# Kernel optimization log

Hardware: AMD Instinct MI355X
Metric: run time of the kernel (lower is better)

## Reference

```python
import jax, jax.numpy as jnp
import numpy as np

B, D, O = 512, 256, 256
H = [512, 1024, 1024]

def _linear_params(key, fan_in, fan_out):
    kw, kb = jax.random.split(key)
    bound = 1.0 / np.sqrt(fan_in)
    W = jax.random.uniform(kw, (fan_out, fan_in), jnp.float32, -bound, bound)
    b = jax.random.uniform(kb, (fan_out,), jnp.float32, -bound, bound)
    return W, b

def setup_inputs() -> dict:
    key = jax.random.key(0)
    ks = jax.random.split(key, 7)
    input_values = jax.random.normal(ks[0], (B, D), jnp.float32)
    nan_flag = jax.random.uniform(ks[1], (B, D), jnp.float32)
    W_in, b_in = _linear_params(ks[2], D, H[0])          # input_layer: nan_flag_dim -> H[0]
    W_h1, b_h1 = _linear_params(ks[3], H[0], H[1])        # hidden layer 1
    W_h2, b_h2 = _linear_params(ks[4], H[1], H[2])        # hidden layer 2
    W_d, b_d = _linear_params(ks[5], H[2], D * O)         # output_branch_dense
    W_b, b_b = _linear_params(ks[6], H[2], O)             # output_branch_bias
    return {"input_values": input_values, "nan_flag": nan_flag, "training": False,
            "W_in": W_in, "b_in": b_in, "W_h1": W_h1, "b_h1": b_h1,
            "W_h2": W_h2, "b_h2": b_h2, "W_d": W_d, "b_d": b_d,
            "W_b": W_b, "b_b": b_b}

def reference(input_values, nan_flag, training, W_in, b_in, W_h1, b_h1, W_h2, b_h2, W_d, b_d, W_b, b_b):
    # training=False: dropout is identity, sample_missing branch skipped (default False)
    x = jax.nn.relu(nan_flag @ W_in.T + b_in)
    x = jax.nn.relu(x @ W_h1.T + b_h1)
    x = jax.nn.relu(x @ W_h2.T + b_h2)
    # per-sample compensation weights [B, D, O] and bias [B, O]
    comp_w = (x @ W_d.T + b_d).reshape(B, D, O)
    comp_b = x @ W_b.T + b_b
    # baddbmm: [B,1,D] @ [B,D,O] + [B,1,O] -> squeeze -> [B,O]
    out = comp_b + jnp.einsum('bd,bdo->bo', input_values, comp_w)
    return out
```

## Files before the change

### kernel.cpp

```cpp
#include <hip/hip_runtime.h>

#define B_  512
#define D_  256
#define O_  256
#define H2_ 1024

typedef __attribute__((ext_vector_type(4))) float  f32x4;
typedef __attribute__((ext_vector_type(8))) short  short8;
typedef __attribute__((ext_vector_type(4))) short  short4v;
typedef unsigned short ushort_t;

union S8u  { short4v v; unsigned u[2]; };
union S16u { short8  v; unsigned u[4]; };

__device__ __forceinline__ unsigned f32_bf16(float x) {
  unsigned u = __builtin_bit_cast(unsigned, x);
  return (u + 0x7fffu + ((u >> 16) & 1u)) >> 16;
}
__device__ __forceinline__ unsigned cvt_pk_bf16(float a, float b) {
  return f32_bf16(a) | (f32_bf16(b) << 16);
}

__device__ __forceinline__ void gload_lds16(const void* g, void* l) {
  __builtin_amdgcn_global_load_lds(
      (const __attribute__((address_space(1))) unsigned*)g,
      (__attribute__((address_space(3))) unsigned*)l, 16, 0, 0);
}

template <int RELU>
__global__ __launch_bounds__(256)
void gemm_bt64(const float* __restrict__ A, const float* __restrict__ Bm,
               const float* __restrict__ bias, float* __restrict__ C,
               int M, int N, int K) {
  __shared__ __align__(16) short As[64][72];
  __shared__ __align__(16) short Bs[64][72];
  const int t    = threadIdx.x;
  const int m0   = blockIdx.y * 64;
  const int n0   = blockIdx.x * 64;
  const int f4c  = t & 15;
  const int rg   = t >> 4;
  const int lane = t & 63;
  const int w    = t >> 6;
  const int wm   = (w & 1) * 32;
  const int wn   = (w >> 1) * 32;
  const int lr   = lane & 15;
  const int lq   = lane >> 4;

  f32x4 acc[2][2];
  #pragma unroll
  for (int i = 0; i < 2; ++i)
    #pragma unroll
    for (int j = 0; j < 2; ++j) acc[i][j] = f32x4{0.f, 0.f, 0.f, 0.f};

  for (int k0 = 0; k0 < K; k0 += 64) {
    #pragma unroll
    for (int j = 0; j < 4; ++j) {
      int r = rg + 16 * j;
      f32x4 av = *(const f32x4*)(A  + (size_t)(m0 + r) * K + k0 + f4c * 4);
      f32x4 bv = *(const f32x4*)(Bm + (size_t)(n0 + r) * K + k0 + f4c * 4);
      S8u sa; sa.u[0] = cvt_pk_bf16(av.x, av.y); sa.u[1] = cvt_pk_bf16(av.z, av.w);
      S8u sb; sb.u[0] = cvt_pk_bf16(bv.x, bv.y); sb.u[1] = cvt_pk_bf16(bv.z, bv.w);
      *(short4v*)&As[r][f4c * 4] = sa.v;
      *(short4v*)&Bs[r][f4c * 4] = sb.v;
    }
    __syncthreads();
    #pragma unroll
    for (int ks = 0; ks < 2; ++ks) {
      short8 a0 = *(const short8*)&As[wm + lr     ][ks * 32 + lq * 8];
      short8 a1 = *(const short8*)&As[wm + 16 + lr][ks * 32 + lq * 8];
      short8 b0 = *(const short8*)&Bs[wn + lr     ][ks * 32 + lq * 8];
      short8 b1 = *(const short8*)&Bs[wn + 16 + lr][ks * 32 + lq * 8];
      acc[0][0] = __builtin_amdgcn_mfma_f32_16x16x32_bf16(a0, b0, acc[0][0], 0, 0, 0);
      acc[0][1] = __builtin_amdgcn_mfma_f32_16x16x32_bf16(a0, b1, acc[0][1], 0, 0, 0);
      acc[1][0] = __builtin_amdgcn_mfma_f32_16x16x32_bf16(a1, b0, acc[1][0], 0, 0, 0);
      acc[1][1] = __builtin_amdgcn_mfma_f32_16x16x32_bf16(a1, b1, acc[1][1], 0, 0, 0);
    }
    __syncthreads();
  }
  #pragma unroll
  for (int mi = 0; mi < 2; ++mi)
    #pragma unroll
    for (int ni = 0; ni < 2; ++ni)
      #pragma unroll
      for (int r = 0; r < 4; ++r) {
        int row = m0 + wm + mi * 16 + lq * 4 + r;
        int col = n0 + wn + ni * 16 + lr;
        float v = acc[mi][ni][r] + bias[col];
        if (RELU) v = fmaxf(v, 0.f);
        C[(size_t)row * N + col] = v;
      }
}

__global__ __launch_bounds__(256)
void cvt_f32_bf16(const float* __restrict__ in, ushort_t* __restrict__ out, int n8) {
  for (size_t i = (size_t)blockIdx.x * 256 + threadIdx.x; i < (size_t)n8;
       i += (size_t)gridDim.x * 256) {
    const float* p = in + i * 8;
    f32x4 v0 = *(const f32x4*)p;
    f32x4 v1 = *(const f32x4*)(p + 4);
    S16u s;
    s.u[0] = cvt_pk_bf16(v0.x, v0.y);
    s.u[1] = cvt_pk_bf16(v0.z, v0.w);
    s.u[2] = cvt_pk_bf16(v1.x, v1.y);
    s.u[3] = cvt_pk_bf16(v1.z, v1.w);
    *(short8*)(out + i * 8) = s.v;
  }
}

__global__ __launch_bounds__(256, 3)
void stage_b5(const ushort_t* __restrict__ x2b, const float* __restrict__ inp,
              const float* __restrict__ Wd, const float* __restrict__ bd,
              float* __restrict__ out) {
  __shared__ __align__(16) ushort_t As[2][128 * 32];
  __shared__ __align__(16) ushort_t Bs[2][128 * 32];
  const int t    = threadIdx.x;
  const int x    = blockIdx.x;
  const int q    = blockIdx.y;
  const int mt   = q & 3;
  const int nb   = (q >> 2) * 8 + x;
  const int d0   = (nb >> 4) * 8;
  const int og   = (nb & 15) * 16;
  const int bm   = mt * 128;
  const int lane = t & 63;
  const int w    = t >> 6;
  const int wm   = (w >> 1) * 64;
  const int wn   = (w & 1) * 64;
  const int lr   = lane & 15;
  const int lq   = lane >> 4;

  const int arow = lane >> 2;
  const int aswz = (lane & 3) ^ ((arow >> 1) & 3);
  const ushort_t* aptr[2];
  #pragma unroll
  for (int c = 0; c < 2; ++c)
    aptr[c] = x2b + (size_t)(bm + w * 32 + c * 16 + arow) * H2_ + aswz * 8;

  const int rr = t >> 1;
  const int hh = t & 1;
  const int wr = (d0 + (rr >> 4)) * O_ + og + (rr & 15);
  const float* bptr = Wd + (size_t)wr * H2_ + hh * 16;
  const int bsw = (rr >> 1) & 3;

  const int sl = (lq ^ ((lr >> 1) & 3)) * 8;

  f32x4 acc[4][4];
  #pragma unroll
  for (int mi = 0; mi < 4; ++mi)
    #pragma unroll
    for (int nj = 0; nj < 4; ++nj) acc[mi][nj] = f32x4{0.f, 0.f, 0.f, 0.f};

  f32x4 breg[4];

  auto stageA = [&](int k, int bf) {
    #pragma unroll
    for (int c = 0; c < 2; ++c)
      gload_lds16(aptr[c] + k * 32, &As[bf][(w * 32 + c * 16) * 32]);
  };
  auto loadB = [&](int k) {
    const float* p = bptr + k * 32;
    breg[0] = *(const f32x4*)p;
    breg[1] = *(const f32x4*)(p + 4);
    breg[2] = *(const f32x4*)(p + 8);
    breg[3] = *(const f32x4*)(p + 12);
  };
  auto writeB = [&](int bf) {
    S16u s0, s1;
    s0.u[0] = cvt_pk_bf16(breg[0].x, breg[0].y);
    s0.u[1] = cvt_pk_bf16(breg[0].z, breg[0].w);
    s0.u[2] = cvt_pk_bf16(breg[1].x, breg[1].y);
    s0.u[3] = cvt_pk_bf16(breg[1].z, breg[1].w);
    s1.u[0] = cvt_pk_bf16(breg[2].x, breg[2].y);
    s1.u[1] = cvt_pk_bf16(breg[2].z, breg[2].w);
    s1.u[2] = cvt_pk_bf16(breg[3].x, breg[3].y);
    s1.u[3] = cvt_pk_bf16(breg[3].z, breg[3].w);
    const int lcg0 = hh * 2;
    *(short8*)&Bs[bf][rr * 32 + (lcg0 ^ bsw) * 8]       = s0.v;
    *(short8*)&Bs[bf][rr * 32 + ((lcg0 + 1) ^ bsw) * 8] = s1.v;
  };

  stageA(0, 0);
  loadB(0);
  asm volatile("s_waitcnt vmcnt(0)" ::: "memory");
  writeB(0);
  asm volatile("s_waitcnt lgkmcnt(0)" ::: "memory");
  __builtin_amdgcn_s_barrier();

  int buf = 0;
  for (int k = 0; k < 32; ++k) {
    if (k < 31) {
      stageA(k + 1, buf ^ 1);
      loadB(k + 1);
    }

    short8 af[4], bfv[4];
    #pragma unroll
    for (int mi = 0; mi < 4; ++mi)
      af[mi] = *(const short8*)&As[buf][(wm + mi * 16 + lr) * 32 + sl];
    #pragma unroll
    for (int nj = 0; nj < 4; ++nj)
      bfv[nj] = *(const short8*)&Bs[buf][(wn + nj * 16 + lr) * 32 + sl];
    #pragma unroll
    for (int mi = 0; mi < 4; ++mi)
      #pragma unroll
      for (int nj = 0; nj < 4; ++nj)
        acc[mi][nj] = __builtin_amdgcn_mfma_f32_16x16x32_bf16(af[mi], bfv[nj],
                                                              acc[mi][nj], 0, 0, 0);

    if (k < 31) {
      asm volatile("s_waitcnt vmcnt(0)" ::: "memory");
      writeB(buf ^ 1);
      asm volatile("s_waitcnt lgkmcnt(0)" ::: "memory");
      __builtin_amdgcn_s_barrier();
      buf ^= 1;
    }
  }

  const int dbase = d0 + (w & 1) * 4;
  const int o     = og + lr;
  float bdv[4];
  #pragma unroll
  for (int nj = 0; nj < 4; ++nj)
    bdv[nj] = bd[(size_t)(dbase + nj) * O_ + o];
  #pragma unroll
  for (int mi = 0; mi < 4; ++mi)
    #pragma unroll
    for (int r = 0; r < 4; ++r) {
      const int row = bm + wm + mi * 16 + lq * 4 + r;
      f32x4 sc = *(const f32x4*)(inp + (size_t)row * D_ + dbase);
      float v = sc.x * (acc[mi][0][r] + bdv[0]) +
                sc.y * (acc[mi][1][r] + bdv[1]) +
                sc.z * (acc[mi][2][r] + bdv[2]) +
                sc.w * (acc[mi][3][r] + bdv[3]);
      atomicAdd(out + (size_t)row * O_ + o, v);
    }
}

extern "C" void kernel_launch(void* const* d_in, const int* in_sizes, int n_in,
                              void* d_out, int out_size, void* d_ws, size_t ws_size,
                              hipStream_t stream) {
  const float* input = (const float*)d_in[0];
  const float* nanf  = (const float*)d_in[1];
  const float* W_in  = (const float*)d_in[3];
  const float* b_in  = (const float*)d_in[4];
  const float* W_h1  = (const float*)d_in[5];
  const float* b_h1  = (const float*)d_in[6];
  const float* W_h2  = (const float*)d_in[7];
  const float* b_h2  = (const float*)d_in[8];
  const float* W_d   = (const float*)d_in[9];
  const float* b_d   = (const float*)d_in[10];
  const float* W_b   = (const float*)d_in[11];
  const float* b_b   = (const float*)d_in[12];
  float* out = (float*)d_out;

  float* x0 = (float*)d_ws;
  float* x1 = x0 + 512 * 512;
  float* x2 = x1 + 512 * 1024;
  ushort_t* x2b = (ushort_t*)(x2 + 512 * 1024);

  gemm_bt64<1><<<dim3(512 / 64, 512 / 64), 256, 0, stream>>>(nanf, W_in, b_in, x0, 512, 512, 256);
  gemm_bt64<1><<<dim3(1024 / 64, 512 / 64), 256, 0, stream>>>(x0, W_h1, b_h1, x1, 512, 1024, 512);
  gemm_bt64<1><<<dim3(1024 / 64, 512 / 64), 256, 0, stream>>>(x1, W_h2, b_h2, x2, 512, 1024, 1024);
  cvt_f32_bf16<<<256, 256, 0, stream>>>(x2, x2b, 512 * 1024 / 8);
  gemm_bt64<0><<<dim3(256 / 64, 512 / 64), 256, 0, stream>>>(x2, W_b, b_b, out, 512, 256, 1024);
  stage_b5<<<dim3(8, 256), 256, 0, stream>>>(x2b, input, W_d, b_d, out);
}
```

Measured before the change: 584.1 us.

## Deepen W_d prefetch and replace atomics with partial buffers plus reduction

The main stage_b kernel now prefetches W_d tiles two k-steps ahead and writes them to LDS before the MFMA loop instead of after it, so global load latency overlaps with compute. The per-element atomicAdd epilogue is replaced by an in-block LDS reduction across the two d-halves, followed by plain stores into 32 partial buffers indexed by d-group. A new reduce_parts kernel sums those partials into the output. Occupancy hint rises from 3 to 4 blocks per SM. The trade-off is extra register pressure from the deeper prefetch, a 16 MB partial workspace, and one more kernel launch.

```diff
diff --git a/kernel.cpp b/kernel.cpp
--- a/kernel.cpp
+++ b/kernel.cpp
@@ -107,10 +107,10 @@
   }
 }
 
-__global__ __launch_bounds__(256, 3)
-void stage_b5(const ushort_t* __restrict__ x2b, const float* __restrict__ inp,
+__global__ __launch_bounds__(256, 4)
+void stage_b6(const ushort_t* __restrict__ x2b, const float* __restrict__ inp,
               const float* __restrict__ Wd, const float* __restrict__ bd,
-              float* __restrict__ out) {
+              float* __restrict__ part) {
   __shared__ __align__(16) ushort_t As[2][128 * 32];
   __shared__ __align__(16) ushort_t Bs[2][128 * 32];
   const int t    = threadIdx.x;
@@ -118,7 +118,8 @@
   const int q    = blockIdx.y;
   const int mt   = q & 3;
   const int nb   = (q >> 2) * 8 + x;
-  const int d0   = (nb >> 4) * 8;
+  const int dg   = nb >> 4;
+  const int d0   = dg * 8;
   const int og   = (nb & 15) * 16;
   const int bm   = mt * 128;
   const int lane = t & 63;
@@ -181,7 +182,9 @@
   stageA(0, 0);
   loadB(0);
   asm volatile("s_waitcnt vmcnt(0)" ::: "memory");
+  __builtin_amdgcn_sched_barrier(0);
   writeB(0);
+  loadB(1);
   asm volatile("s_waitcnt lgkmcnt(0)" ::: "memory");
   __builtin_amdgcn_s_barrier();
 
@@ -189,7 +192,10 @@
   for (int k = 0; k < 32; ++k) {
     if (k < 31) {
       stageA(k + 1, buf ^ 1);
-      loadB(k + 1);
+      asm volatile("s_waitcnt vmcnt(2)" ::: "memory");
+      __builtin_amdgcn_sched_barrier(0);
+      writeB(buf ^ 1);
+      if (k < 30) loadB(k + 2);
     }
 
     short8 af[4], bfv[4];
@@ -207,13 +213,14 @@
                                                               acc[mi][nj], 0, 0, 0);
 
     if (k < 31) {
-      asm volatile("s_waitcnt vmcnt(0)" ::: "memory");
-      writeB(buf ^ 1);
+      if (k < 30) { asm volatile("s_waitcnt vmcnt(4)" ::: "memory"); }
+      else        { asm volatile("s_waitcnt vmcnt(0)" ::: "memory"); }
       asm volatile("s_waitcnt lgkmcnt(0)" ::: "memory");
       __builtin_amdgcn_s_barrier();
       buf ^= 1;
     }
   }
+  __builtin_amdgcn_sched_barrier(0);
 
   const int dbase = d0 + (w & 1) * 4;
   const int o     = og + lr;
@@ -221,18 +228,54 @@
   #pragma unroll
   for (int nj = 0; nj < 4; ++nj)
     bdv[nj] = bd[(size_t)(dbase + nj) * O_ + o];
+
+  float v[4][4];
   #pragma unroll
   for (int mi = 0; mi < 4; ++mi)
     #pragma unroll
     for (int r = 0; r < 4; ++r) {
       const int row = bm + wm + mi * 16 + lq * 4 + r;
       f32x4 sc = *(const f32x4*)(inp + (size_t)row * D_ + dbase);
-      float v = sc.x * (acc[mi][0][r] + bdv[0]) +
-                sc.y * (acc[mi][1][r] + bdv[1]) +
-                sc.z * (acc[mi][2][r] + bdv[2]) +
-                sc.w * (acc[mi][3][r] + bdv[3]);
-      atomicAdd(out + (size_t)row * O_ + o, v);
-    }
+      v[mi][r] = sc.x * (acc[mi][0][r] + bdv[0]) +
+                 sc.y * (acc[mi][1][r] + bdv[1]) +
+                 sc.z * (acc[mi][2][r] + bdv[2]) +
+                 sc.w * (acc[mi][3][r] + bdv[3]);
+    }
+
+  __syncthreads();
+  float* lf = (float*)As;
+  if (w & 1) {
+    #pragma unroll
+    for (int mi = 0; mi < 4; ++mi)
+      #pragma unroll
+      for (int r = 0; r < 4; ++r) {
+        const int rl = wm + mi * 16 + lq * 4 + r;
+        lf[rl * 17 + lr] = v[mi][r];
+      }
+  }
+  __syncthreads();
+  if (!(w & 1)) {
+    float* pb = part + (size_t)dg * (B_ * O_);
+    #pragma unroll
+    for (int mi = 0; mi < 4; ++mi)
+      #pragma unroll
+      for (int r = 0; r < 4; ++r) {
+        const int rl = wm + mi * 16 + lq * 4 + r;
+        pb[(size_t)(bm + rl) * O_ + o] = v[mi][r] + lf[rl * 17 + lr];
+      }
+  }
+}
+
+__global__ __launch_bounds__(256)
+void reduce_parts(const float* __restrict__ part, float* __restrict__ out) {
+  const int b = blockIdx.x;
+  const int o = threadIdx.x;
+  const size_t idx = (size_t)b * O_ + o;
+  float s = 0.f;
+  #pragma unroll 8
+  for (int j = 0; j < 32; ++j)
+    s += part[(size_t)j * (B_ * O_) + idx];
+  out[idx] += s;
 }
 
 extern "C" void kernel_launch(void* const* d_in, const int* in_sizes, int n_in,
@@ -256,11 +299,13 @@
   float* x1 = x0 + 512 * 512;
   float* x2 = x1 + 512 * 1024;
   ushort_t* x2b = (ushort_t*)(x2 + 512 * 1024);
+  float* part = (float*)((char*)d_ws + 8ull * 1024 * 1024);
 
   gemm_bt64<1><<<dim3(512 / 64, 512 / 64), 256, 0, stream>>>(nanf, W_in, b_in, x0, 512, 512, 256);
   gemm_bt64<1><<<dim3(1024 / 64, 512 / 64), 256, 0, stream>>>(x0, W_h1, b_h1, x1, 512, 1024, 512);
   gemm_bt64<1><<<dim3(1024 / 64, 512 / 64), 256, 0, stream>>>(x1, W_h2, b_h2, x2, 512, 1024, 1024);
   cvt_f32_bf16<<<256, 256, 0, stream>>>(x2, x2b, 512 * 1024 / 8);
   gemm_bt64<0><<<dim3(256 / 64, 512 / 64), 256, 0, stream>>>(x2, W_b, b_b, out, 512, 256, 1024);
-  stage_b5<<<dim3(8, 256), 256, 0, stream>>>(x2b, input, W_d, b_d, out);
-}
+  stage_b6<<<dim3(8, 256), 256, 0, stream>>>(x2b, input, W_d, b_d, part);
+  reduce_parts<<<512, 256, 0, stream>>>(part, out);
+}
```

After: 568.4 us. 1.03x faster.
